# Kernel tuning notes

Hardware: AMD Instinct MI355X
Metric: run time of the kernel (lower is better)

Reference implementation:

```python
import jax, jax.numpy as jnp
import numpy as np

INPUT_DIM, HIDDEN_DIM, OUTPUT_DIM, NUM_LAYERS = 128, 512, 128, 2
B, T = 32, 2048


def setup_inputs() -> dict:
    key = jax.random.key(0)
    ks = jax.random.split(key, 11)
    s_in = 1.0 / np.sqrt(HIDDEN_DIM)
    inp = {"x": jax.random.normal(ks[0], (B, T, INPUT_DIM), dtype=jnp.float32)}
    # layer 0 (input_dim -> hidden), layer 1 (hidden -> hidden); PyTorch gate order i,f,g,o
    inp["w_ih0"] = jax.random.uniform(ks[1], (4 * HIDDEN_DIM, INPUT_DIM), minval=-s_in, maxval=s_in)
    inp["w_hh0"] = jax.random.uniform(ks[2], (4 * HIDDEN_DIM, HIDDEN_DIM), minval=-s_in, maxval=s_in)
    inp["b_ih0"] = jax.random.uniform(ks[3], (4 * HIDDEN_DIM,), minval=-s_in, maxval=s_in)
    inp["b_hh0"] = jax.random.uniform(ks[4], (4 * HIDDEN_DIM,), minval=-s_in, maxval=s_in)
    inp["w_ih1"] = jax.random.uniform(ks[5], (4 * HIDDEN_DIM, HIDDEN_DIM), minval=-s_in, maxval=s_in)
    inp["w_hh1"] = jax.random.uniform(ks[6], (4 * HIDDEN_DIM, HIDDEN_DIM), minval=-s_in, maxval=s_in)
    inp["b_ih1"] = jax.random.uniform(ks[7], (4 * HIDDEN_DIM,), minval=-s_in, maxval=s_in)
    inp["b_hh1"] = jax.random.uniform(ks[8], (4 * HIDDEN_DIM,), minval=-s_in, maxval=s_in)
    inp["fc_w"] = jax.random.uniform(ks[9], (OUTPUT_DIM, HIDDEN_DIM), minval=-s_in, maxval=s_in)
    inp["fc_b"] = jax.random.uniform(ks[10], (OUTPUT_DIM,), minval=-s_in, maxval=s_in)
    return inp


def _lstm_layer(x, w_ih, w_hh, b_ih, b_hh):
    # x: [B, T, D] -> hidden states [B, T, H], final (h, c) each [B, H]
    b, t, _ = x.shape
    h4 = w_hh.shape[0]
    H = h4 // 4
    # precompute input projections for all timesteps (one big GEMM)
    x_proj = jnp.einsum('btd,gd->btg', x, w_ih) + b_ih + b_hh  # [B, T, 4H]

    def step(carry, xt):
        h, c = carry
        gates = xt + h @ w_hh.T  # [B, 4H]
        i, f, g, o = jnp.split(gates, 4, axis=-1)
        i = jax.nn.sigmoid(i)
        f = jax.nn.sigmoid(f)
        g = jnp.tanh(g)
        o = jax.nn.sigmoid(o)
        c = f * c + i * g
        h = o * jnp.tanh(c)
        return (h, c), h

    init = (jnp.zeros((b, H), x.dtype), jnp.zeros((b, H), x.dtype))
    (h_n, c_n), hs = jax.lax.scan(step, init, jnp.swapaxes(x_proj, 0, 1))
    return jnp.swapaxes(hs, 0, 1), h_n, c_n


def reference(x, w_ih0, w_hh0, b_ih0, b_hh0, w_ih1, w_hh1, b_ih1, b_hh1, fc_w, fc_b):
    out0, h0, c0 = _lstm_layer(x, w_ih0, w_hh0, b_ih0, b_hh0)
    out1, h1, c1 = _lstm_layer(out0, w_ih1, w_hh1, b_ih1, b_hh1)
    h_n = jnp.stack([h0, h1])  # [L, B, H]
    c_n = jnp.stack([c0, c1])  # [L, B, H]
    # fc(relu(.)) applied once over all (batch, time) -- collapses the Python loop
    output = jnp.einsum('bth,oh->bto', jax.nn.relu(out1), fc_w) + fc_b  # [B, T, O]
    hidden = jnp.einsum('lbh,oh->lbo', jax.nn.relu(h_n), fc_w) + fc_b   # [L, B, O]
    return jnp.squeeze(output), hidden, c_n
```

## Files before the change

kernel.cpp:

```cpp
#include <hip/hip_runtime.h>

typedef unsigned int u32;
typedef unsigned short u16;
typedef unsigned long long u64;

#define T_STEPS 2048
#define BATCH   32
#define HID     512
#define INDIM   128
#define OUTD    128
#define NG      2048
#define L0_WGS  64
#define L1_WGS  64
#define FC_WGS  4
#define NWG     (L0_WGS + L1_WGS + FC_WGS)
#define BH      (BATCH * HID)
#define SLOT_Q  4096

#define HID_OFF 8388608
#define CN_OFF  8396800

#define WS_FLAGS   0
#define WS_H0RING  16384
#define WS_H1RING  (WS_H0RING + 131072)
#define WS_BIAS0   (WS_H1RING + 131072)
#define WS_BIAS1   (WS_BIAS0 + 8192)
#define WS_WFC     (WS_BIAS1 + 8192)
#define WS_WL0     (WS_WFC + 131072)
#define WS_WL1     (WS_WL0 + 2621440)
#define WS_XBF     (WS_WL1 + 4194304)
#define WS_H0DEEP  (WS_XBF + 16777216)
#define WS_H1DEEP  (WS_H0DEEP + 67141632)
#define WS_DEEPEND (WS_H1DEEP + 67141632)

typedef __bf16 bf16x8 __attribute__((ext_vector_type(8)));
typedef float  f32x4  __attribute__((ext_vector_type(4)));
typedef unsigned int u32x4 __attribute__((ext_vector_type(4)));

__device__ __forceinline__ u16 f2bf(float f) {
    u32 u = __float_as_uint(f);
    u32 r = u + 0x7FFFu + ((u >> 16) & 1u);
    return (u16)(r >> 16);
}

union UB2 { u32x4 u; bf16x8 b; };
__device__ __forceinline__ bf16x8 as_bf(u32x4 u) { UB2 x; x.u = u; return x.b; }

__device__ __forceinline__ u32 relu2(u32 u) {
    u32 lo = (u & 0x8000u)     ? 0u : (u & 0xFFFFu);
    u32 hi = (u & 0x80000000u) ? 0u : (u & 0xFFFF0000u);
    return lo | hi;
}

__device__ __forceinline__ u32x4 ld16_llc(const void* p) {
    u32x4 r;
    asm volatile("global_load_dwordx4 %0, %1, off sc0 sc1"
                 : "=v"(r) : "v"(p) : "memory");
    return r;
}
__device__ __forceinline__ u32x4 ld16_l2(const void* p) {
    u32x4 r;
    asm volatile("global_load_dwordx4 %0, %1, off sc0"
                 : "=v"(r) : "v"(p) : "memory");
    return r;
}
__device__ __forceinline__ void wait_vm0() {
    asm volatile("s_waitcnt vmcnt(0)" ::: "memory");
    __builtin_amdgcn_sched_barrier(0);
}
__device__ __forceinline__ void vm0() {
    asm volatile("s_waitcnt vmcnt(0)" ::: "memory");
}


__global__ void k_zero(u32* dst, int n) {
    int i = blockIdx.x * blockDim.x + threadIdx.x;
    if (i < n) dst[i] = 0u;
}

__global__ void k_bias(const float* __restrict__ bih0, const float* __restrict__ bhh0,
                       const float* __restrict__ bih1, const float* __restrict__ bhh1,
                       float* __restrict__ bias0, float* __restrict__ bias1) {
    int i = blockIdx.x * blockDim.x + threadIdx.x;
    if (i < NG) {
        int orig = (i & 3) * HID + (i >> 2);
        bias0[i] = bih0[orig] + bhh0[orig];
        bias1[i] = bih1[orig] + bhh1[orig];
    }
}

__global__ void k_xconv(const float* __restrict__ x, u16* __restrict__ xbf) {
    int i = blockIdx.x * blockDim.x + threadIdx.x;
    float4 v = reinterpret_cast<const float4*>(x)[i];
    u32 lo = (u32)f2bf(v.x) | ((u32)f2bf(v.y) << 16);
    u32 hi = (u32)f2bf(v.z) | ((u32)f2bf(v.w) << 16);
    reinterpret_cast<uint2*>(xbf)[i] = make_uint2(lo, hi);
}

__global__ void k_wconv(const float* __restrict__ wih0, const float* __restrict__ whh0,
                        const float* __restrict__ wih1, const float* __restrict__ whh1,
                        const float* __restrict__ fcw,
                        u16* __restrict__ wl0, u16* __restrict__ wl1, u16* __restrict__ wfc) {
    int i = blockIdx.x * blockDim.x + threadIdx.x;
    if (i < 64 * 20480) {
        int wg = i / 20480, r = i % 20480;
        int ks = r / 1024, kb = (r % 1024) / 256, n = (r % 256) / 8, j = r % 8;
        int k = ks * 32 + kb * 8 + j;
        int p = wg * 32 + n;
        int orig = (p & 3) * HID + (p >> 2);
        float v = (k < HID) ? whh0[orig * HID + k] : wih0[orig * INDIM + (k - HID)];
        wl0[i] = f2bf(v);
        return;
    }
    int i1 = i - 64 * 20480;
    if (i1 < 64 * 32768) {
        int wg = i1 / 32768, r = i1 % 32768;
        int ks = r / 1024, kb = (r % 1024) / 256, n = (r % 256) / 8, j = r % 8;
        int k = ks * 32 + kb * 8 + j;
        int p = wg * 32 + n;
        int orig = (p & 3) * HID + (p >> 2);
        float v = (k < HID) ? wih1[orig * HID + k] : whh1[orig * HID + (k - HID)];
        wl1[i1] = f2bf(v);
        return;
    }
    int i2 = i1 - 64 * 32768;
    if (i2 < 4 * 16384) {
        int wg = i2 / 16384, r = i2 % 16384;
        int ks = r / 1024, kb = (r % 1024) / 256, n = (r % 256) / 8, j = r % 8;
        int k = ks * 32 + kb * 8 + j;
        int o = wg * 32 + n;
        wfc[i2] = f2bf(fcw[o * HID + k]);
    }
}


__global__ __launch_bounds__(256, 1)
void k_lstm(const u16* __restrict__ xbf,
            const u16* __restrict__ wl0g, const u16* __restrict__ wl1g, const u16* __restrict__ wfcg,
            const float* __restrict__ bias0, const float* __restrict__ bias1, const float* __restrict__ fcb,
            u16* __restrict__ h0ring, u16* __restrict__ h1ring,
            u32* __restrict__ flags, float* __restrict__ dout, const int deep)
{
    __shared__ u16 wlds[32768];
    __shared__ __align__(16) u64 hq[2][4096];
    const int tid  = threadIdx.x;
    const int lane = tid & 63;
    const int wv   = tid >> 6;
    const int mt   = wv >> 1;
    const int nt   = wv & 1;
    const int ci   = lane & 15;
    const int quad = lane >> 4;
    const int wg   = blockIdx.x;

    int role, rwg;
    if      (wg < L0_WGS)           { role = 0; rwg = wg; }
    else if (wg < L0_WGS + L1_WGS)  { role = 1; rwg = wg - L0_WGS; }
    else                            { role = 2; rwg = wg - L0_WGS - L1_WGS; }

    u32* flagL0 = flags;
    u32* flagL1 = flags + 64 * 16;
    u32* flagFC = flags + 128 * 16;
    u32* myflag = flags + wg * 16;

    {
        const u16* src = (role == 0) ? (wl0g + rwg * 20480)
                       : (role == 1) ? (wl1g + rwg * 32768)
                                     : (wfcg + rwg * 16384);
        const int n4 = (role == 0) ? 2560 : (role == 1) ? 4096 : 2048;
        uint4* d4 = reinterpret_cast<uint4*>(wlds);
        const uint4* s4 = reinterpret_cast<const uint4*>(src);
        for (int i = tid; i < n4; i += 256) d4[i] = s4[i];
    }
    __syncthreads();

    const bf16x8* wp = reinterpret_cast<const bf16x8*>(wlds);
    const int wbase  = quad * 32 + nt * 16 + ci;
    const int pcol   = rwg * 32 + nt * 16 + ci;
    const int gateid = pcol & 3;
    const float bias = (role == 0) ? bias0[pcol] : (role == 1) ? bias1[pcol] : fcb[pcol];
    const int brow0  = mt * 16 + quad * 4;
    const int arow   = mt * 16 + ci;
    const int jidx   = pcol >> 2;
    const int hswz   = arow & 7;

    float cst[4] = {0.f, 0.f, 0.f, 0.f};

    auto spin = [&](u32* f, int target) {
        if (target > 0)
            while ((int)__hip_atomic_load(f, __ATOMIC_RELAXED, __HIP_MEMORY_SCOPE_AGENT) < target)
                __builtin_amdgcn_s_sleep(1);
    };

    auto slotQ = [&](u16* ring, int t_h) -> u64* {
        long idx = deep ? (long)(t_h + 1) : (long)(t_h & 3);
        return reinterpret_cast<u64*>(ring) + idx * SLOT_Q;
    };

    auto scat = [&](int buf, int c, u32x4 b) {
        int g0  = 2 * c;
        int rw_ = g0 >> 6, nt_ = (g0 >> 5) & 1, mt_ = (g0 >> 4) & 1;
        int qd  = (g0 >> 2) & 3, c0 = g0 & 3;
        int row = mt_ * 16 + qd * 4 + c0;
        int u   = rw_ * 2 + nt_;
        int p   = u >> 1, ub = u & 1;
        hq[buf][ row      * 128 + (((p ^ ( row      & 7)) << 1) | ub)] = (u64)b[0] | ((u64)b[1] << 32);
        hq[buf][(row + 1) * 128 + (((p ^ ((row + 1) & 7)) << 1) | ub)] = (u64)b[2] | ((u64)b[3] << 32);
    };

    auto stage1 = [&](const u64* sq, int buf) {
        u32x4 b[8];
        if (deep) {
            #pragma unroll
            for (int r = 0; r < 8; ++r) b[r] = ld16_l2(sq + 2 * (tid + r * 256));
        } else {
            #pragma unroll
            for (int r = 0; r < 8; ++r) b[r] = ld16_llc(sq + 2 * (tid + r * 256));
        }
        wait_vm0();
        #pragma unroll
        for (int r = 0; r < 8; ++r) scat(buf, tid + r * 256, b[r]);
    };
    auto stage2 = [&](const u64* s0, const u64* s1) {
        u32x4 b0[8], b1[8];
        if (deep) {
            #pragma unroll
            for (int r = 0; r < 8; ++r) b0[r] = ld16_l2(s0 + 2 * (tid + r * 256));
            #pragma unroll
            for (int r = 0; r < 8; ++r) b1[r] = ld16_l2(s1 + 2 * (tid + r * 256));
        } else {
            #pragma unroll
            for (int r = 0; r < 8; ++r) b0[r] = ld16_llc(s0 + 2 * (tid + r * 256));
            #pragma unroll
            for (int r = 0; r < 8; ++r) b1[r] = ld16_llc(s1 + 2 * (tid + r * 256));
        }
        wait_vm0();
        #pragma unroll
        for (int r = 0; r < 8; ++r) scat(0, tid + r * 256, b0[r]);
        #pragma unroll
        for (int r = 0; r < 8; ++r) scat(1, tid + r * 256, b1[r]);
    };

    auto epi = [&](const f32x4& acc, u64* sq) {
        float ga[4], hv[4];
        #pragma unroll
        for (int r = 0; r < 4; ++r) {
            float g  = acc[r] + bias;
            float sv = 1.0f / (1.0f + __expf(-g));
            float tv = 1.0f - 2.0f / (__expf(2.0f * g) + 1.0f);
            ga[r] = (gateid == 2) ? tv : sv;
        }
        const int bl = lane & ~3;
        #pragma unroll
        for (int r = 0; r < 4; ++r) {
            float iv = __shfl(ga[r], bl + 0);
            float fv = __shfl(ga[r], bl + 1);
            float gv = __shfl(ga[r], bl + 2);
            float ov = __shfl(ga[r], bl + 3);
            float cn = fv * cst[r] + iv * gv;
            cst[r] = cn;
            hv[r] = ov * (1.0f - 2.0f / (__expf(2.0f * cn) + 1.0f));
        }
        u32 lo = 0, hi = 0;
        #pragma unroll
        for (int r = 0; r < 4; ++r) {
            float c0 = __shfl(hv[r], (quad << 4) + 0);
            float c1 = __shfl(hv[r], (quad << 4) + 4);
            float c2 = __shfl(hv[r], (quad << 4) + 8);
            float c3 = __shfl(hv[r], (quad << 4) + 12);
            if (ci == r) {
                lo = (u32)f2bf(c0) | ((u32)f2bf(c1) << 16);
                hi = (u32)f2bf(c2) | ((u32)f2bf(c3) << 16);
            }
        }
        if (ci < 4) {
            u64* dst = sq + rwg * 64 + nt * 32 + mt * 16 + quad * 4 + ci;
            u64 val = (u64)lo | ((u64)hi << 32);
            __hip_atomic_store(dst, val, __ATOMIC_RELAXED, __HIP_MEMORY_SCOPE_AGENT);
        }
    };

    #define HMFMA16S(BUF, KSOFF)                                                 \
        _Pragma("unroll")                                                        \
        for (int _k = 0; _k < 16; ++_k) {                                        \
          u32x4 _hv = *reinterpret_cast<const u32x4*>(                           \
              &hq[BUF][arow * 128 + (((_k * 4 + quad) ^ hswz) << 1)]);           \
          bf16x8 _bv = wp[wbase + (_k + (KSOFF)) * 128];                         \
          if (_k & 1) accB = __builtin_amdgcn_mfma_f32_16x16x32_bf16(as_bf(_hv), _bv, accB, 0, 0, 0); \
          else        accA = __builtin_amdgcn_mfma_f32_16x16x32_bf16(as_bf(_hv), _bv, accA, 0, 0, 0); \
        }

    auto fcTileS = [&](int buf) -> f32x4 {
        f32x4 accA = {0.f,0.f,0.f,0.f}, accB = {0.f,0.f,0.f,0.f};
        #pragma unroll
        for (int ks = 0; ks < 16; ++ks) {
            u32x4 v = *reinterpret_cast<const u32x4*>(
                &hq[buf][arow * 128 + (((ks * 4 + quad) ^ hswz) << 1)]);
            v[0] = relu2(v[0]); v[1] = relu2(v[1]); v[2] = relu2(v[2]); v[3] = relu2(v[3]);
            bf16x8 bv = wp[wbase + ks * 128];
            if (ks & 1) accB = __builtin_amdgcn_mfma_f32_16x16x32_bf16(as_bf(v), bv, accB, 0, 0, 0);
            else        accA = __builtin_amdgcn_mfma_f32_16x16x32_bf16(as_bf(v), bv, accA, 0, 0, 0);
        }
        return accA + accB;
    };

    if (role == 0) {
        u32* pf = (tid < 64) ? (flagL0 + tid * 16)
                : (!deep && tid < 128) ? (flagL1 + (tid - 64) * 16) : nullptr;
        const int po = (tid < 64) ? 0 : -3;
        for (int t = 0; t < T_STEPS; ++t) {
            const u16* xA = xbf + (arow * T_STEPS + t) * INDIM + quad * 8;
            f32x4 accA = {0.f, 0.f, 0.f, 0.f}, accB = {0.f, 0.f, 0.f, 0.f};
            u32x4 xv[4];
            #pragma unroll
            for (int k4 = 0; k4 < 4; ++k4) xv[k4] = *reinterpret_cast<const u32x4*>(xA + k4 * 32);
            #pragma unroll
            for (int k4 = 0; k4 < 4; ++k4) {
                bf16x8 bv = wp[wbase + (16 + k4) * 128];
                if (k4 & 1) accB = __builtin_amdgcn_mfma_f32_16x16x32_bf16(as_bf(xv[k4]), bv, accB, 0, 0, 0);
                else        accA = __builtin_amdgcn_mfma_f32_16x16x32_bf16(as_bf(xv[k4]), bv, accA, 0, 0, 0);
            }
            if (pf) spin(pf, t + po);
            __syncthreads();
            stage1(slotQ(h0ring, t - 1), 0);
            __syncthreads();
            HMFMA16S(0, 0);
            epi(accA + accB, slotQ(h0ring, t));
            vm0();
            __syncthreads();
            if (tid == 0)
                __hip_atomic_store(myflag, (u32)(t + 1), __ATOMIC_RELAXED, __HIP_MEMORY_SCOPE_AGENT);
        }
    } else if (role == 1) {
        u32* pf = (tid < 64)  ? (flagL0 + tid * 16)
                : (tid < 128) ? (flagL1 + (tid - 64) * 16)
                : (!deep && tid < 132) ? (flagFC + (tid - 128) * 16) : nullptr;
        const int po = (tid < 64) ? 1 : (tid < 128) ? 0 : -3;
        for (int t = 0; t < T_STEPS; ++t) {
            if (pf) spin(pf, t + po);
            __syncthreads();
            stage2(slotQ(h0ring, t),
                   slotQ(h1ring, t - 1));
            __syncthreads();
            f32x4 accA = {0.f, 0.f, 0.f, 0.f}, accB = {0.f, 0.f, 0.f, 0.f};
            HMFMA16S(0, 0);
            HMFMA16S(1, 16);
            epi(accA + accB, slotQ(h1ring, t));
            vm0();
            __syncthreads();
            if (tid == 0)
                __hip_atomic_store(myflag, (u32)(t + 1), __ATOMIC_RELAXED, __HIP_MEMORY_SCOPE_AGENT);
        }
    } else {
        u32* pf = (tid < 64) ? (flagL1 + tid * 16) : nullptr;
        for (int t = 0; t < T_STEPS; ++t) {
            if (pf) spin(pf, t + 1);
            __syncthreads();
            stage1(slotQ(h1ring, t), 0);
            __syncthreads();
            f32x4 acc = fcTileS(0);
            #pragma unroll
            for (int r = 0; r < 4; ++r)
                dout[((brow0 + r) * T_STEPS + t) * OUTD + pcol] = acc[r] + bias;
            __syncthreads();
            if (tid == 0)
                __hip_atomic_store(myflag, (u32)(t + 1), __ATOMIC_RELAXED, __HIP_MEMORY_SCOPE_AGENT);
        }
        stage1(slotQ(h0ring, T_STEPS - 1), 1);
        __syncthreads();
        f32x4 hh1 = fcTileS(0);
        f32x4 hh0 = fcTileS(1);
        #pragma unroll
        for (int r = 0; r < 4; ++r)
            dout[HID_OFF + (brow0 + r) * OUTD + pcol] = hh0[r] + bias;
        #pragma unroll
        for (int r = 0; r < 4; ++r)
            dout[HID_OFF + (BATCH + brow0 + r) * OUTD + pcol] = hh1[r] + bias;
    }

    if (role <= 1 && (ci & 3) == 0) {
        #pragma unroll
        for (int r = 0; r < 4; ++r)
            dout[CN_OFF + (role * BATCH + brow0 + r) * HID + jidx] = cst[r];
    }
}


extern "C" void kernel_launch(void* const* d_in, const int* in_sizes, int n_in,
                              void* d_out, int out_size, void* d_ws, size_t ws_size,
                              hipStream_t stream) {
    const float* x    = (const float*)d_in[0];
    const float* wih0 = (const float*)d_in[1];
    const float* whh0 = (const float*)d_in[2];
    const float* bih0 = (const float*)d_in[3];
    const float* bhh0 = (const float*)d_in[4];
    const float* wih1 = (const float*)d_in[5];
    const float* whh1 = (const float*)d_in[6];
    const float* bih1 = (const float*)d_in[7];
    const float* bhh1 = (const float*)d_in[8];
    const float* fcw  = (const float*)d_in[9];
    const float* fcb  = (const float*)d_in[10];

    char* ws = (char*)d_ws;
    u32*  flags = (u32*)(ws + WS_FLAGS);
    float* b0   = (float*)(ws + WS_BIAS0);
    float* b1   = (float*)(ws + WS_BIAS1);
    u16*  wfc   = (u16*)(ws + WS_WFC);
    u16*  wl0   = (u16*)(ws + WS_WL0);
    u16*  wl1   = (u16*)(ws + WS_WL1);
    u16*  xbf   = (u16*)(ws + WS_XBF);
    float* dout = (float*)d_out;

    const int deep = (ws_size >= (size_t)WS_DEEPEND) ? 1 : 0;
    u16* h0r = deep ? (u16*)(ws + WS_H0DEEP) : (u16*)(ws + WS_H0RING);
    u16* h1r = deep ? (u16*)(ws + WS_H1DEEP) : (u16*)(ws + WS_H1RING);

    if (deep) {
        k_zero<<<16, 256, 0, stream>>>((u32*)ws, 4096);
        k_zero<<<32, 256, 0, stream>>>((u32*)(ws + WS_H0DEEP), 8192);
        k_zero<<<32, 256, 0, stream>>>((u32*)(ws + WS_H1DEEP), 8192);
    } else {
        k_zero<<<272, 256, 0, stream>>>((u32*)ws, 69632);
    }
    k_bias<<<8, 256, 0, stream>>>(bih0, bhh0, bih1, bhh1, b0, b1);
    k_xconv<<<8192, 256, 0, stream>>>(x, xbf);
    k_wconv<<<13568, 256, 0, stream>>>(wih0, whh0, wih1, whh1, fcw, wl0, wl1, wfc);
    k_lstm<<<NWG, 256, 0, stream>>>(xbf, wl0, wl1, wfc, b0, b1, fcb,
                                    h0r, h1r, flags, dout, deep);
}
```

Before: 9.192 ms.

## Replace per-workgroup flag polling with rotating arrival counters and pad LDS rows

In deep mode, the 64 per-producer flags each consumer workgroup polled are replaced by eight rotating atomic counters per layer. Every producer increments a counter once per step, and a single thread per consumer waits until that counter reaches 64 times the round number. This is meant to cut the polling traffic and the number of waiting lanes in the cross-workgroup handoff, at the price of atomic contention on one shared counter. The LDS staging row stride also grows from 128 to 130 u64 to reduce bank conflicts.

```diff
diff --git a/kernel.cpp b/kernel.cpp
--- a/kernel.cpp
+++ b/kernel.cpp
@@ -16,6 +16,7 @@
 #define NWG     (L0_WGS + L1_WGS + FC_WGS)
 #define BH      (BATCH * HID)
 #define SLOT_Q  4096
+#define HQS     130
 
 #define HID_OFF 8388608
 #define CN_OFF  8396800
@@ -32,6 +33,9 @@
 #define WS_H0DEEP  (WS_XBF + 16777216)
 #define WS_H1DEEP  (WS_H0DEEP + 67141632)
 #define WS_DEEPEND (WS_H1DEEP + 67141632)
+
+#define F_CNT0  3584
+#define F_CNT1  3712
 
 typedef __bf16 bf16x8 __attribute__((ext_vector_type(8)));
 typedef float  f32x4  __attribute__((ext_vector_type(4)));
@@ -142,7 +146,7 @@
             u32* __restrict__ flags, float* __restrict__ dout, const int deep)
 {
     __shared__ u16 wlds[32768];
-    __shared__ __align__(16) u64 hq[2][4096];
+    __shared__ __align__(16) u64 hq[2][32 * HQS];
     const int tid  = threadIdx.x;
     const int lane = tid & 63;
     const int wv   = tid >> 6;
@@ -161,6 +165,8 @@
     u32* flagL1 = flags + 64 * 16;
     u32* flagFC = flags + 128 * 16;
     u32* myflag = flags + wg * 16;
+    u32* cnt0   = flags + F_CNT0;
+    u32* cnt1   = flags + F_CNT1;
 
     {
         const u16* src = (role == 0) ? (wl0g + rwg * 20480)
@@ -190,6 +196,11 @@
             while ((int)__hip_atomic_load(f, __ATOMIC_RELAXED, __HIP_MEMORY_SCOPE_AGENT) < target)
                 __builtin_amdgcn_s_sleep(1);
     };
+    auto spinC = [&](u32* f, u32 target) {
+        while (__hip_atomic_load(f, __ATOMIC_RELAXED, __HIP_MEMORY_SCOPE_AGENT) < target)
+            __builtin_amdgcn_s_sleep(1);
+    };
+    auto expv = [&](int t, u32 n) -> u32 { return n * (u32)((t >> 3) + 1); };
 
     auto slotQ = [&](u16* ring, int t_h) -> u64* {
         long idx = deep ? (long)(t_h + 1) : (long)(t_h & 3);
@@ -203,8 +214,8 @@
         int row = mt_ * 16 + qd * 4 + c0;
         int u   = rw_ * 2 + nt_;
         int p   = u >> 1, ub = u & 1;
-        hq[buf][ row      * 128 + (((p ^ ( row      & 7)) << 1) | ub)] = (u64)b[0] | ((u64)b[1] << 32);
-        hq[buf][(row + 1) * 128 + (((p ^ ((row + 1) & 7)) << 1) | ub)] = (u64)b[2] | ((u64)b[3] << 32);
+        hq[buf][ row      * HQS + (((p ^ ( row      & 7)) << 1) | ub)] = (u64)b[0] | ((u64)b[1] << 32);
+        hq[buf][(row + 1) * HQS + (((p ^ ((row + 1) & 7)) << 1) | ub)] = (u64)b[2] | ((u64)b[3] << 32);
     };
 
     auto stage1 = [&](const u64* sq, int buf) {
@@ -283,7 +294,7 @@
         _Pragma("unroll")                                                        \
         for (int _k = 0; _k < 16; ++_k) {                                        \
           u32x4 _hv = *reinterpret_cast<const u32x4*>(                           \
-              &hq[BUF][arow * 128 + (((_k * 4 + quad) ^ hswz) << 1)]);           \
+              &hq[BUF][arow * HQS + (((_k * 4 + quad) ^ hswz) << 1)]);           \
           bf16x8 _bv = wp[wbase + (_k + (KSOFF)) * 128];                         \
           if (_k & 1) accB = __builtin_amdgcn_mfma_f32_16x16x32_bf16(as_bf(_hv), _bv, accB, 0, 0, 0); \
           else        accA = __builtin_amdgcn_mfma_f32_16x16x32_bf16(as_bf(_hv), _bv, accA, 0, 0, 0); \
@@ -294,7 +305,7 @@
         #pragma unroll
         for (int ks = 0; ks < 16; ++ks) {
             u32x4 v = *reinterpret_cast<const u32x4*>(
-                &hq[buf][arow * 128 + (((ks * 4 + quad) ^ hswz) << 1)]);
+                &hq[buf][arow * HQS + (((ks * 4 + quad) ^ hswz) << 1)]);
             v[0] = relu2(v[0]); v[1] = relu2(v[1]); v[2] = relu2(v[2]); v[3] = relu2(v[3]);
             bf16x8 bv = wp[wbase + ks * 128];
             if (ks & 1) accB = __builtin_amdgcn_mfma_f32_16x16x32_bf16(as_bf(v), bv, accB, 0, 0, 0);
@@ -304,7 +315,7 @@
     };
 
     if (role == 0) {
-        u32* pf = (tid < 64) ? (flagL0 + tid * 16)
+        u32* pf = (!deep && tid < 64) ? (flagL0 + tid * 16)
                 : (!deep && tid < 128) ? (flagL1 + (tid - 64) * 16) : nullptr;
         const int po = (tid < 64) ? 0 : -3;
         for (int t = 0; t < T_STEPS; ++t) {
@@ -319,7 +330,9 @@
                 if (k4 & 1) accB = __builtin_amdgcn_mfma_f32_16x16x32_bf16(as_bf(xv[k4]), bv, accB, 0, 0, 0);
                 else        accA = __builtin_amdgcn_mfma_f32_16x16x32_bf16(as_bf(xv[k4]), bv, accA, 0, 0, 0);
             }
-            if (pf) spin(pf, t + po);
+            if (deep) {
+                if (tid == 0 && t > 0) spinC(cnt0 + ((t - 1) & 7) * 16, expv(t - 1, 64));
+            } else if (pf) spin(pf, t + po);
             __syncthreads();
             stage1(slotQ(h0ring, t - 1), 0);
             __syncthreads();
@@ -327,16 +340,21 @@
             epi(accA + accB, slotQ(h0ring, t));
             vm0();
             __syncthreads();
-            if (tid == 0)
-                __hip_atomic_store(myflag, (u32)(t + 1), __ATOMIC_RELAXED, __HIP_MEMORY_SCOPE_AGENT);
+            if (tid == 0) {
+                if (deep) atomicAdd(cnt0 + (t & 7) * 16, 1u);
+                else __hip_atomic_store(myflag, (u32)(t + 1), __ATOMIC_RELAXED, __HIP_MEMORY_SCOPE_AGENT);
+            }
         }
     } else if (role == 1) {
-        u32* pf = (tid < 64)  ? (flagL0 + tid * 16)
-                : (tid < 128) ? (flagL1 + (tid - 64) * 16)
+        u32* pf = (!deep && tid < 64)  ? (flagL0 + tid * 16)
+                : (!deep && tid < 128) ? (flagL1 + (tid - 64) * 16)
                 : (!deep && tid < 132) ? (flagFC + (tid - 128) * 16) : nullptr;
         const int po = (tid < 64) ? 1 : (tid < 128) ? 0 : -3;
         for (int t = 0; t < T_STEPS; ++t) {
-            if (pf) spin(pf, t + po);
+            if (deep) {
+                if (tid == 0)               spinC(cnt0 + (t & 7) * 16, expv(t, 64));
+                else if (tid == 64 && t > 0) spinC(cnt1 + ((t - 1) & 7) * 16, expv(t - 1, 64));
+            } else if (pf) spin(pf, t + po);
             __syncthreads();
             stage2(slotQ(h0ring, t),
                    slotQ(h1ring, t - 1));
@@ -347,13 +365,17 @@
             epi(accA + accB, slotQ(h1ring, t));
             vm0();
             __syncthreads();
-            if (tid == 0)
-                __hip_atomic_store(myflag, (u32)(t + 1), __ATOMIC_RELAXED, __HIP_MEMORY_SCOPE_AGENT);
+            if (tid == 0) {
+                if (deep) atomicAdd(cnt1 + (t & 7) * 16, 1u);
+                else __hip_atomic_store(myflag, (u32)(t + 1), __ATOMIC_RELAXED, __HIP_MEMORY_SCOPE_AGENT);
+            }
         }
     } else {
-        u32* pf = (tid < 64) ? (flagL1 + tid * 16) : nullptr;
+        u32* pf = (!deep && tid < 64) ? (flagL1 + tid * 16) : nullptr;
         for (int t = 0; t < T_STEPS; ++t) {
-            if (pf) spin(pf, t + 1);
+            if (deep) {
+                if (tid == 0) spinC(cnt1 + (t & 7) * 16, expv(t, 64));
+            } else if (pf) spin(pf, t + 1);
             __syncthreads();
             stage1(slotQ(h1ring, t), 0);
             __syncthreads();
@@ -362,7 +384,7 @@
             for (int r = 0; r < 4; ++r)
                 dout[((brow0 + r) * T_STEPS + t) * OUTD + pcol] = acc[r] + bias;
             __syncthreads();
-            if (tid == 0)
+            if (tid == 0 && !deep)
                 __hip_atomic_store(myflag, (u32)(t + 1), __ATOMIC_RELAXED, __HIP_MEMORY_SCOPE_AGENT);
         }
         stage1(slotQ(h0ring, T_STEPS - 1), 1);
```

Result: slower. 16.11 ms (+75.3%).
